# Performance work log

Hardware: AMD Instinct MI355X
Metric: run time of the kernel (lower is better)

## Reference

```python
import jax, jax.numpy as jnp
import numpy as np

HEADS = 8
DIM_HEAD = 64
SCALE = DIM_HEAD ** -0.5


def setup_inputs() -> dict:
    key = jax.random.key(0)
    k1, k2, k3, k4 = jax.random.split(key, 4)
    b, dim, l = 4, 512, 2048
    hidden = HEADS * DIM_HEAD  # 512
    x = jax.random.normal(k1, (b, dim, l), dtype=jnp.float32)
    w_qkv = jax.random.normal(k2, (3 * hidden, dim), dtype=jnp.float32) * (dim ** -0.5)
    w_out = jax.random.normal(k3, (dim, hidden), dtype=jnp.float32) * (hidden ** -0.5)
    b_out = jax.random.normal(k4, (dim,), dtype=jnp.float32) * 0.01
    return {"x": x, "w_qkv": w_qkv, "w_out": w_out, "b_out": b_out}


def reference(x, w_qkv, w_out, b_out):
    b, c, l = x.shape
    h, d = HEADS, DIM_HEAD
    # 1x1 Conv1d == channel matmul: [3*hidden, c] x [b, c, l] -> [b, 3*hidden, l]
    qkv = jnp.einsum('oc,bcl->bol', w_qkv, x)
    q, k, v = jnp.split(qkv, 3, axis=1)
    # 'b (h d) l -> b h d l'
    q = q.reshape(b, h, d, l) * SCALE
    k = k.reshape(b, h, d, l)
    v = v.reshape(b, h, d, l)
    sim = jnp.einsum('bhdi,bhdj->bhij', q, k)          # [b, h, l, l]
    attn = jax.nn.softmax(sim, axis=-1)
    out = jnp.einsum('bhij,bhdj->bhid', attn, v)       # [b, h, l, d]
    # 'b h l d -> b (h d) l'
    out = out.transpose(0, 1, 3, 2).reshape(b, h * d, l)
    return jnp.einsum('oc,bcl->bol', w_out, out) + b_out[None, :, None]
```

## Files before the change

kernel.cpp:

```cpp
#include <hip/hip_runtime.h>

#define L_SEQ 2048
#define KDIM  512

typedef __attribute__((ext_vector_type(8))) short short8v;
typedef __attribute__((ext_vector_type(4))) float f32x4;

static __device__ __forceinline__ short f2b(float f) {
    union { float f; unsigned u; } v; v.f = f;
    unsigned r = v.u + 0x7fffu + ((v.u >> 16) & 1u);
    return (short)(r >> 16);
}

static __device__ __forceinline__ float fast_exp2(float x) {
#if __has_builtin(__builtin_amdgcn_exp2f)
    return __builtin_amdgcn_exp2f(x);
#else
    return exp2f(x);
#endif
}

static __device__ __forceinline__ void gl2lds16(const short* g, short* l) {
    __builtin_amdgcn_global_load_lds(
        (const __attribute__((address_space(1))) unsigned*)g,
        (__attribute__((address_space(3))) unsigned*)l,
        16, 0, 0);
}

__global__ __launch_bounds__(256) void prep(
    const float* __restrict__ wq, const float* __restrict__ wo,
    const float* __restrict__ x,
    short* __restrict__ wqb, short* __restrict__ wob, short* __restrict__ xT)
{
    __shared__ __align__(16) float T[64 * 72];
    const int t = threadIdx.x;
    int bid = blockIdx.x;

    if (bid < 1024) {
        const int i = bid * 256 + t;
        const int NQ = 1536 * 512 / 4;
        float4 v;
        if (i < NQ) v = ((const float4*)wq)[i];
        else        v = ((const float4*)wo)[i - NQ];
        short4 s;
        s.x = f2b(v.x); s.y = f2b(v.y); s.z = f2b(v.z); s.w = f2b(v.w);
        if (i < NQ) ((short4*)wqb)[i] = s;
        else        ((short4*)wob)[i - NQ] = s;
        return;
    }
    bid -= 1024;
    const int l0 = (bid & 31) * 64;
    const int c0 = ((bid >> 5) & 7) * 64;
    const int b  = bid >> 8;

#pragma unroll
    for (int j = 0; j < 4; ++j) {
        const int idx = j * 256 + t;
        const int row = idx >> 4, c4 = idx & 15;
        const float4 v = *(const float4*)&x[((size_t)b * KDIM + c0 + row) * L_SEQ + l0 + c4 * 4];
        *(float4*)&T[row * 72 + c4 * 4] = v;
    }
    __syncthreads();

#pragma unroll
    for (int j = 0; j < 2; ++j) {
        const int idx = j * 256 + t;
        const int l = idx >> 3, ch = idx & 7;
        short8v s;
#pragma unroll
        for (int e = 0; e < 8; ++e)
            s[e] = f2b(T[(ch * 8 + e) * 72 + l]);
        *(short8v*)&xT[((size_t)b * L_SEQ + l0 + l) * KDIM + c0 + ch * 8] = s;
    }
}

template<int EPI>
__global__ __launch_bounds__(256) void gemm_bt(
    const short* __restrict__ Ag, const short* __restrict__ Bbase,
    const float* __restrict__ bias,
    short* __restrict__ Qws, short* __restrict__ Kws, short* __restrict__ Vws,
    float* __restrict__ Cout)
{
    constexpr int TO   = (EPI == 0) ? 128 : 64;
    constexpr int WO   = TO / 2;
    constexpr int NI   = WO / 16;
    constexpr int CA   = TO * 64 * 2 / 1024;
    constexpr int CB   = 16;
    constexpr int CPW  = (CA + CB) / 4;
    constexpr int SMEM = (EPI == 0) ? 34816 : 24576;

    const int bz = blockIdx.z;
    const int o0 = blockIdx.y * TO;
    const int l0 = blockIdx.x * 128;
    const short* Bg = Bbase + (size_t)bz * L_SEQ * KDIM;

    __shared__ __align__(16) char smem[SMEM];
    short* sA = (short*)smem;
    short* sB = (short*)(smem + TO * 64 * 2);

    const int t    = threadIdx.x;
    const int w    = t >> 6;
    const int lane = t & 63;
    const int quad = lane >> 4;
    const int l16  = lane & 15;
    const int wo   = (w & 1) * WO;
    const int wl   = (w >> 1) * 64;

    f32x4 acc[NI][4];
#pragma unroll
    for (int i = 0; i < NI; ++i)
#pragma unroll
        for (int n = 0; n < 4; ++n) acc[i][n] = (f32x4){0,0,0,0};

    const int lrow = lane >> 3;
    const int lcol = (lane & 7) * 8;

    for (int k0 = 0; k0 < KDIM; k0 += 64) {
#pragma unroll
        for (int p = 0; p < CPW; ++p) {
            const int cid = w * CPW + p;
            if (cid < CA) {
                const int row = cid * 8 + lrow;
                gl2lds16(Ag + (size_t)(o0 + row) * KDIM + k0 + lcol, sA + cid * 512);
            } else {
                const int row = (cid - CA) * 8 + lrow;
                gl2lds16(Bg + (size_t)(l0 + row) * KDIM + k0 + lcol, sB + (cid - CA) * 512);
            }
        }
        __syncthreads();

#pragma unroll
        for (int ks = 0; ks < 2; ++ks) {
            short8v af[NI], bf[4];
#pragma unroll
            for (int i = 0; i < NI; ++i)
                af[i] = *(const short8v*)&sA[(wo + i * 16 + l16) * 64 + ks * 32 + quad * 8];
#pragma unroll
            for (int n = 0; n < 4; ++n)
                bf[n] = *(const short8v*)&sB[(wl + n * 16 + l16) * 64 + ks * 32 + quad * 8];
#pragma unroll
            for (int i = 0; i < NI; ++i)
#pragma unroll
                for (int n = 0; n < 4; ++n)
                    acc[i][n] = __builtin_amdgcn_mfma_f32_16x16x32_bf16(af[i], bf[n], acc[i][n], 0, 0, 0);
        }
        __syncthreads();
    }

    if (EPI == 0) {
        const int type  = o0 >> 9;
        const int local = o0 & 511;
        const int bh0   = bz * 8 + (local >> 6);
        const float sc  = (type == 0) ? 0.18033688011112042f : 1.0f;
        short* T = (short*)smem;

        if (type == 2) {
#pragma unroll
            for (int i = 0; i < NI; ++i)
#pragma unroll
                for (int n = 0; n < 4; ++n)
#pragma unroll
                    for (int r = 0; r < 4; ++r)
                        T[(wo + i * 16 + quad * 4 + r) * 136 + wl + n * 16 + l16] =
                            f2b(acc[i][n][r]);
            __syncthreads();
#pragma unroll
            for (int p = 0; p < 8; ++p) {
                const int idx = p * 256 + t;
                const int o = idx >> 4, c = idx & 15;
                const float4 v = *(const float4*)&T[o * 136 + c * 8];
                short* dst = Vws + ((size_t)(bh0 + (o >> 6)) * 64 + (o & 63)) * L_SEQ + l0 + c * 8;
                *(float4*)dst = v;
            }
        } else {
#pragma unroll
            for (int i = 0; i < NI; ++i)
#pragma unroll
                for (int n = 0; n < 4; ++n) {
                    short4 s;
                    s.x = f2b(acc[i][n][0] * sc);
                    s.y = f2b(acc[i][n][1] * sc);
                    s.z = f2b(acc[i][n][2] * sc);
                    s.w = f2b(acc[i][n][3] * sc);
                    *(short4*)&T[(wl + n * 16 + l16) * 136 + wo + i * 16 + quad * 4] = s;
                }
            __syncthreads();
            short* base = (type == 0) ? Qws : Kws;
#pragma unroll
            for (int p = 0; p < 8; ++p) {
                const int idx = p * 256 + t;
                const int l = idx >> 4, c = idx & 15;
                const float4 v = *(const float4*)&T[l * 136 + c * 8];
                short* dst = base + ((size_t)(bh0 + (c >> 3)) * L_SEQ + l0 + l) * 64 + (c & 7) * 8;
                *(float4*)dst = v;
            }
        }
    } else {
        float* Cb = Cout + (size_t)bz * KDIM * L_SEQ;
#pragma unroll
        for (int i = 0; i < NI; ++i) {
            const int o = o0 + wo + i * 16 + quad * 4;
            float bv[4];
#pragma unroll
            for (int r = 0; r < 4; ++r) bv[r] = bias[o + r];
#pragma unroll
            for (int n = 0; n < 4; ++n) {
                const int l = l0 + wl + n * 16 + l16;
#pragma unroll
                for (int r = 0; r < 4; ++r)
                    Cb[(size_t)(o + r) * L_SEQ + l] = acc[i][n][r] + bv[r];
            }
        }
    }
}

__global__ __launch_bounds__(256) void attn_mfma(
    const short* __restrict__ Qws, const short* __restrict__ Kws,
    const short* __restrict__ Vws, short* __restrict__ ao)
{
    const int bh = blockIdx.x & 31;
    const int b  = bh >> 3;
    const int h  = bh & 7;
    const int i0 = (blockIdx.x >> 5) * 128;

    __shared__ __align__(16) char smem[36864];
    short* Kld = (short*)smem;
    short* Vld = (short*)(smem + 9216);
    short* Pld = (short*)(smem + 18432);
    float* Old = (float*)smem;

    const int t    = threadIdx.x;
    const int w    = t >> 6;
    const int lane = t & 63;
    const int quad = lane >> 4;
    const int l16  = lane & 15;

    const short* Qb = Qws + (size_t)bh * L_SEQ * 64;
    const short* Kb = Kws + (size_t)bh * L_SEQ * 64;
    const short* Vb = Vws + (size_t)bh * 64 * L_SEQ;

    short8v qa[2][2];
#pragma unroll
    for (int hh = 0; hh < 2; ++hh) {
        const short* qrow = Qb + (size_t)(i0 + w * 32 + hh * 16 + l16) * 64 + quad * 8;
        qa[hh][0] = *(const short8v*)qrow;
        qa[hh][1] = *(const short8v*)(qrow + 32);
    }

    f32x4 oacc[2][4];
#pragma unroll
    for (int hh = 0; hh < 2; ++hh)
#pragma unroll
        for (int n = 0; n < 4; ++n) oacc[hh][n] = (f32x4){0,0,0,0};
    float rsum[2] = {0.f, 0.f};
    short* Pw = Pld + w * 32 * 72;

    const int r = t >> 2, c = t & 3;

    for (int j0 = 0; j0 < L_SEQ; j0 += 64) {
        {
            const float4 k0 = *(const float4*)(Kb + (size_t)(j0 + r) * 64 + c * 16);
            const float4 k1 = *(const float4*)(Kb + (size_t)(j0 + r) * 64 + c * 16 + 8);
            const float4 v0 = *(const float4*)(Vb + (size_t)r * L_SEQ + j0 + c * 16);
            const float4 v1 = *(const float4*)(Vb + (size_t)r * L_SEQ + j0 + c * 16 + 8);
            *(float4*)&Kld[r * 72 + c * 16]     = k0;
            *(float4*)&Kld[r * 72 + c * 16 + 8] = k1;
            *(float4*)&Vld[r * 72 + c * 16]     = v0;
            *(float4*)&Vld[r * 72 + c * 16 + 8] = v1;
        }
        __syncthreads();

        f32x4 sacc[2][4];
#pragma unroll
        for (int hh = 0; hh < 2; ++hh)
#pragma unroll
            for (int n = 0; n < 4; ++n) sacc[hh][n] = (f32x4){0,0,0,0};
#pragma unroll
        for (int n = 0; n < 4; ++n) {
            short8v kf0 = *(const short8v*)&Kld[(n * 16 + l16) * 72 + quad * 8];
            short8v kf1 = *(const short8v*)&Kld[(n * 16 + l16) * 72 + 32 + quad * 8];
#pragma unroll
            for (int hh = 0; hh < 2; ++hh) {
                sacc[hh][n] = __builtin_amdgcn_mfma_f32_16x16x32_bf16(kf0, qa[hh][0], sacc[hh][n], 0, 0, 0);
                sacc[hh][n] = __builtin_amdgcn_mfma_f32_16x16x32_bf16(kf1, qa[hh][1], sacc[hh][n], 0, 0, 0);
            }
        }

#pragma unroll
        for (int hh = 0; hh < 2; ++hh)
#pragma unroll
            for (int n = 0; n < 4; ++n) {
                const float p0 = fast_exp2(sacc[hh][n][0]);
                const float p1 = fast_exp2(sacc[hh][n][1]);
                const float p2 = fast_exp2(sacc[hh][n][2]);
                const float p3 = fast_exp2(sacc[hh][n][3]);
                rsum[hh] += (p0 + p1) + (p2 + p3);
                uint2 pv;
                pv.x = __builtin_amdgcn_perm(__float_as_uint(p1), __float_as_uint(p0), 0x07060302u);
                pv.y = __builtin_amdgcn_perm(__float_as_uint(p3), __float_as_uint(p2), 0x07060302u);
                *(uint2*)&Pw[(hh * 16 + l16) * 72 + n * 16 + quad * 4] = pv;
            }

        short8v pa[2][2];
#pragma unroll
        for (int hh = 0; hh < 2; ++hh) {
            pa[hh][0] = *(const short8v*)&Pw[(hh * 16 + l16) * 72 + quad * 8];
            pa[hh][1] = *(const short8v*)&Pw[(hh * 16 + l16) * 72 + 32 + quad * 8];
        }
#pragma unroll
        for (int n = 0; n < 4; ++n) {
            short8v vf0 = *(const short8v*)&Vld[(n * 16 + l16) * 72 + quad * 8];
            short8v vf1 = *(const short8v*)&Vld[(n * 16 + l16) * 72 + 32 + quad * 8];
#pragma unroll
            for (int hh = 0; hh < 2; ++hh) {
                oacc[hh][n] = __builtin_amdgcn_mfma_f32_16x16x32_bf16(pa[hh][0], vf0, oacc[hh][n], 0, 0, 0);
                oacc[hh][n] = __builtin_amdgcn_mfma_f32_16x16x32_bf16(pa[hh][1], vf1, oacc[hh][n], 0, 0, 0);
            }
        }
        __syncthreads();
    }

    float inv[2];
#pragma unroll
    for (int hh = 0; hh < 2; ++hh) {
        rsum[hh] += __shfl_xor(rsum[hh], 16, 64);
        rsum[hh] += __shfl_xor(rsum[hh], 32, 64);
        inv[hh] = 1.0014f / rsum[hh];
    }

#pragma unroll
    for (int hh = 0; hh < 2; ++hh)
#pragma unroll
        for (int rr = 0; rr < 4; ++rr) {
            const float iv = __shfl(inv[hh], quad * 4 + rr, 64);
#pragma unroll
            for (int n = 0; n < 4; ++n)
                Old[(w * 32 + hh * 16 + quad * 4 + rr) * 68 + n * 16 + l16] =
                    oacc[hh][n][rr] * iv;
        }
    __syncthreads();
#pragma unroll
    for (int p = 0; p < 8; ++p) {
        const int idx = p * 256 + t;
        const int i = idx >> 4, c4 = idx & 15;
        const float4 v = *(const float4*)&Old[i * 68 + c4 * 4];
        short4 s;
        s.x = f2b(v.x); s.y = f2b(v.y); s.z = f2b(v.z); s.w = f2b(v.w);
        *(short4*)&ao[((size_t)b * L_SEQ + i0 + i) * KDIM + h * 64 + c4 * 4] = s;
    }
}

extern "C" void kernel_launch(void* const* d_in, const int* in_sizes, int n_in,
                              void* d_out, int out_size, void* d_ws, size_t ws_size,
                              hipStream_t stream)
{
    const float* x     = (const float*)d_in[0];
    const float* w_qkv = (const float*)d_in[1];
    const float* w_out = (const float*)d_in[2];
    const float* b_out = (const float*)d_in[3];
    float* out = (float*)d_out;

    char* ws = (char*)d_ws;
    short* xT    = (short*)ws;                      ws += (size_t)4 * L_SEQ * KDIM * 2;
    short* wq_bf = (short*)ws;                      ws += (size_t)1536 * 512 * 2;
    short* wo_bf = (short*)ws;                      ws += (size_t)512 * 512 * 2;
    short* Qws   = (short*)ws;                      ws += (size_t)32 * L_SEQ * 64 * 2;
    short* Kws   = (short*)ws;                      ws += (size_t)32 * L_SEQ * 64 * 2;
    short* Vws   = (short*)ws;                      ws += (size_t)32 * L_SEQ * 64 * 2;
    short* ao    = (short*)ws;

    dim3 blk(256);
    prep       <<<dim3(2048), blk, 0, stream>>>(w_qkv, w_out, x, wq_bf, wo_bf, xT);
    gemm_bt<0> <<<dim3(16, 12, 4), blk, 0, stream>>>(wq_bf, xT, nullptr, Qws, Kws, Vws, nullptr);
    attn_mfma  <<<dim3(512), blk, 0, stream>>>(Qws, Kws, Vws, ao);
    gemm_bt<1> <<<dim3(16, 8, 4), blk, 0, stream>>>(wo_bf, ao, b_out, nullptr, nullptr, nullptr, out);
}
```

Before: 168.1 us.

## Double-buffer K/V tiles and split attention block into eight 16-row waves

The attention kernel now uses 512 threads, with each wave owning 16 query rows instead of 32. K/V tiles are double-buffered in LDS, and the next tile is prefetched into registers while the current one is computed, which leaves one barrier per iteration. This aims to hide global load latency and raise wave-level parallelism per block. The cost is more LDS per block and less K/V fragment reuse per wave, which may lower occupancy.

```diff
diff --git a/kernel.cpp b/kernel.cpp
--- a/kernel.cpp
+++ b/kernel.cpp
@@ -214,7 +214,7 @@
     }
 }
 
-__global__ __launch_bounds__(256) void attn_mfma(
+__global__ __launch_bounds__(512) void attn_mfma(
     const short* __restrict__ Qws, const short* __restrict__ Kws,
     const short* __restrict__ Vws, short* __restrict__ ao)
 {
@@ -223,10 +223,8 @@
     const int h  = bh & 7;
     const int i0 = (blockIdx.x >> 5) * 128;
 
-    __shared__ __align__(16) char smem[36864];
-    short* Kld = (short*)smem;
-    short* Vld = (short*)(smem + 9216);
-    short* Pld = (short*)(smem + 18432);
+    __shared__ __align__(16) char smem[55296];
+    short* Pld = (short*)(smem + 36864);
     float* Old = (float*)smem;
 
     const int t    = threadIdx.x;
@@ -239,109 +237,101 @@
     const short* Kb = Kws + (size_t)bh * L_SEQ * 64;
     const short* Vb = Vws + (size_t)bh * 64 * L_SEQ;
 
-    short8v qa[2][2];
-#pragma unroll
-    for (int hh = 0; hh < 2; ++hh) {
-        const short* qrow = Qb + (size_t)(i0 + w * 32 + hh * 16 + l16) * 64 + quad * 8;
-        qa[hh][0] = *(const short8v*)qrow;
-        qa[hh][1] = *(const short8v*)(qrow + 32);
-    }
-
-    f32x4 oacc[2][4];
-#pragma unroll
-    for (int hh = 0; hh < 2; ++hh)
-#pragma unroll
-        for (int n = 0; n < 4; ++n) oacc[hh][n] = (f32x4){0,0,0,0};
-    float rsum[2] = {0.f, 0.f};
-    short* Pw = Pld + w * 32 * 72;
-
-    const int r = t >> 2, c = t & 3;
-
-    for (int j0 = 0; j0 < L_SEQ; j0 += 64) {
-        {
-            const float4 k0 = *(const float4*)(Kb + (size_t)(j0 + r) * 64 + c * 16);
-            const float4 k1 = *(const float4*)(Kb + (size_t)(j0 + r) * 64 + c * 16 + 8);
-            const float4 v0 = *(const float4*)(Vb + (size_t)r * L_SEQ + j0 + c * 16);
-            const float4 v1 = *(const float4*)(Vb + (size_t)r * L_SEQ + j0 + c * 16 + 8);
-            *(float4*)&Kld[r * 72 + c * 16]     = k0;
-            *(float4*)&Kld[r * 72 + c * 16 + 8] = k1;
-            *(float4*)&Vld[r * 72 + c * 16]     = v0;
-            *(float4*)&Vld[r * 72 + c * 16 + 8] = v1;
+    short8v qa0, qa1;
+    {
+        const short* qrow = Qb + (size_t)(i0 + w * 16 + l16) * 64 + quad * 8;
+        qa0 = *(const short8v*)qrow;
+        qa1 = *(const short8v*)(qrow + 32);
+    }
+
+    f32x4 oacc[4];
+#pragma unroll
+    for (int n = 0; n < 4; ++n) oacc[n] = (f32x4){0,0,0,0};
+    float rsum = 0.f;
+    short* Pw = Pld + w * 16 * 72;
+
+    const int r = t >> 3, c = t & 7;
+
+    {
+        short* K0 = (short*)smem;
+        short* V0 = (short*)(smem + 9216);
+        const float4 k0 = *(const float4*)(Kb + (size_t)r * 64 + c * 8);
+        const float4 v0 = *(const float4*)(Vb + (size_t)r * L_SEQ + c * 8);
+        *(float4*)&K0[r * 72 + c * 8] = k0;
+        *(float4*)&V0[r * 72 + c * 8] = v0;
+    }
+    __syncthreads();
+
+    for (int jt = 0; jt < L_SEQ / 64; ++jt) {
+        const int j0 = jt * 64;
+        short* Kc = (short*)(smem + (jt & 1) * 18432);
+        short* Vc = (short*)(smem + (jt & 1) * 18432 + 9216);
+        const bool more = (jt + 1 < L_SEQ / 64);
+
+        float4 nk, nv;
+        if (more) {
+            nk = *(const float4*)(Kb + (size_t)(j0 + 64 + r) * 64 + c * 8);
+            nv = *(const float4*)(Vb + (size_t)r * L_SEQ + j0 + 64 + c * 8);
+        }
+
+        f32x4 sacc[4];
+#pragma unroll
+        for (int n = 0; n < 4; ++n) sacc[n] = (f32x4){0,0,0,0};
+#pragma unroll
+        for (int n = 0; n < 4; ++n) {
+            const short8v kf0 = *(const short8v*)&Kc[(n * 16 + l16) * 72 + quad * 8];
+            const short8v kf1 = *(const short8v*)&Kc[(n * 16 + l16) * 72 + 32 + quad * 8];
+            sacc[n] = __builtin_amdgcn_mfma_f32_16x16x32_bf16(kf0, qa0, sacc[n], 0, 0, 0);
+            sacc[n] = __builtin_amdgcn_mfma_f32_16x16x32_bf16(kf1, qa1, sacc[n], 0, 0, 0);
+        }
+
+#pragma unroll
+        for (int n = 0; n < 4; ++n) {
+            const float p0 = fast_exp2(sacc[n][0]);
+            const float p1 = fast_exp2(sacc[n][1]);
+            const float p2 = fast_exp2(sacc[n][2]);
+            const float p3 = fast_exp2(sacc[n][3]);
+            rsum += (p0 + p1) + (p2 + p3);
+            uint2 pv;
+            pv.x = __builtin_amdgcn_perm(__float_as_uint(p1), __float_as_uint(p0), 0x07060302u);
+            pv.y = __builtin_amdgcn_perm(__float_as_uint(p3), __float_as_uint(p2), 0x07060302u);
+            *(uint2*)&Pw[l16 * 72 + n * 16 + quad * 4] = pv;
+        }
+
+        const short8v pa0 = *(const short8v*)&Pw[l16 * 72 + quad * 8];
+        const short8v pa1 = *(const short8v*)&Pw[l16 * 72 + 32 + quad * 8];
+#pragma unroll
+        for (int n = 0; n < 4; ++n) {
+            const short8v vf0 = *(const short8v*)&Vc[(n * 16 + l16) * 72 + quad * 8];
+            const short8v vf1 = *(const short8v*)&Vc[(n * 16 + l16) * 72 + 32 + quad * 8];
+            oacc[n] = __builtin_amdgcn_mfma_f32_16x16x32_bf16(pa0, vf0, oacc[n], 0, 0, 0);
+            oacc[n] = __builtin_amdgcn_mfma_f32_16x16x32_bf16(pa1, vf1, oacc[n], 0, 0, 0);
+        }
+
+        if (more) {
+            short* Kn = (short*)(smem + ((jt & 1) ^ 1) * 18432);
+            short* Vn = (short*)(smem + ((jt & 1) ^ 1) * 18432 + 9216);
+            *(float4*)&Kn[r * 72 + c * 8] = nk;
+            *(float4*)&Vn[r * 72 + c * 8] = nv;
         }
         __syncthreads();
-
-        f32x4 sacc[2][4];
-#pragma unroll
-        for (int hh = 0; hh < 2; ++hh)
-#pragma unroll
-            for (int n = 0; n < 4; ++n) sacc[hh][n] = (f32x4){0,0,0,0};
-#pragma unroll
-        for (int n = 0; n < 4; ++n) {
-            short8v kf0 = *(const short8v*)&Kld[(n * 16 + l16) * 72 + quad * 8];
-            short8v kf1 = *(const short8v*)&Kld[(n * 16 + l16) * 72 + 32 + quad * 8];
-#pragma unroll
-            for (int hh = 0; hh < 2; ++hh) {
-                sacc[hh][n] = __builtin_amdgcn_mfma_f32_16x16x32_bf16(kf0, qa[hh][0], sacc[hh][n], 0, 0, 0);
-                sacc[hh][n] = __builtin_amdgcn_mfma_f32_16x16x32_bf16(kf1, qa[hh][1], sacc[hh][n], 0, 0, 0);
-            }
-        }
-
-#pragma unroll
-        for (int hh = 0; hh < 2; ++hh)
-#pragma unroll
-            for (int n = 0; n < 4; ++n) {
-                const float p0 = fast_exp2(sacc[hh][n][0]);
-                const float p1 = fast_exp2(sacc[hh][n][1]);
-                const float p2 = fast_exp2(sacc[hh][n][2]);
-                const float p3 = fast_exp2(sacc[hh][n][3]);
-                rsum[hh] += (p0 + p1) + (p2 + p3);
-                uint2 pv;
-                pv.x = __builtin_amdgcn_perm(__float_as_uint(p1), __float_as_uint(p0), 0x07060302u);
-                pv.y = __builtin_amdgcn_perm(__float_as_uint(p3), __float_as_uint(p2), 0x07060302u);
-                *(uint2*)&Pw[(hh * 16 + l16) * 72 + n * 16 + quad * 4] = pv;
-            }
-
-        short8v pa[2][2];
-#pragma unroll
-        for (int hh = 0; hh < 2; ++hh) {
-            pa[hh][0] = *(const short8v*)&Pw[(hh * 16 + l16) * 72 + quad * 8];
-            pa[hh][1] = *(const short8v*)&Pw[(hh * 16 + l16) * 72 + 32 + quad * 8];
-        }
-#pragma unroll
-        for (int n = 0; n < 4; ++n) {
-            short8v vf0 = *(const short8v*)&Vld[(n * 16 + l16) * 72 + quad * 8];
-            short8v vf1 = *(const short8v*)&Vld[(n * 16 + l16) * 72 + 32 + quad * 8];
-#pragma unroll
-            for (int hh = 0; hh < 2; ++hh) {
-                oacc[hh][n] = __builtin_amdgcn_mfma_f32_16x16x32_bf16(pa[hh][0], vf0, oacc[hh][n], 0, 0, 0);
-                oacc[hh][n] = __builtin_amdgcn_mfma_f32_16x16x32_bf16(pa[hh][1], vf1, oacc[hh][n], 0, 0, 0);
-            }
-        }
-        __syncthreads();
-    }
-
-    float inv[2];
-#pragma unroll
-    for (int hh = 0; hh < 2; ++hh) {
-        rsum[hh] += __shfl_xor(rsum[hh], 16, 64);
-        rsum[hh] += __shfl_xor(rsum[hh], 32, 64);
-        inv[hh] = 1.0014f / rsum[hh];
-    }
-
-#pragma unroll
-    for (int hh = 0; hh < 2; ++hh)
-#pragma unroll
-        for (int rr = 0; rr < 4; ++rr) {
-            const float iv = __shfl(inv[hh], quad * 4 + rr, 64);
-#pragma unroll
-            for (int n = 0; n < 4; ++n)
-                Old[(w * 32 + hh * 16 + quad * 4 + rr) * 68 + n * 16 + l16] =
-                    oacc[hh][n][rr] * iv;
-        }
+    }
+
+    rsum += __shfl_xor(rsum, 16, 64);
+    rsum += __shfl_xor(rsum, 32, 64);
+    const float inv = 1.0014f / rsum;
+
+#pragma unroll
+    for (int rr = 0; rr < 4; ++rr) {
+        const float iv = __shfl(inv, quad * 4 + rr, 64);
+#pragma unroll
+        for (int n = 0; n < 4; ++n)
+            Old[(w * 16 + quad * 4 + rr) * 68 + n * 16 + l16] = oacc[n][rr] * iv;
+    }
     __syncthreads();
 #pragma unroll
-    for (int p = 0; p < 8; ++p) {
-        const int idx = p * 256 + t;
+    for (int p = 0; p < 4; ++p) {
+        const int idx = p * 512 + t;
         const int i = idx >> 4, c4 = idx & 15;
         const float4 v = *(const float4*)&Old[i * 68 + c4 * 4];
         short4 s;
@@ -372,6 +362,6 @@
     dim3 blk(256);
     prep       <<<dim3(2048), blk, 0, stream>>>(w_qkv, w_out, x, wq_bf, wo_bf, xT);
     gemm_bt<0> <<<dim3(16, 12, 4), blk, 0, stream>>>(wq_bf, xT, nullptr, Qws, Kws, Vws, nullptr);
-    attn_mfma  <<<dim3(512), blk, 0, stream>>>(Qws, Kws, Vws, ao);
+    attn_mfma  <<<dim3(512), dim3(512), 0, stream>>>(Qws, Kws, Vws, ao);
     gemm_bt<1> <<<dim3(16, 8, 4), blk, 0, stream>>>(wo_bf, ao, b_out, nullptr, nullptr, nullptr, out);
 }
```

New measurement: 168.8 us. About the same (+0.4%).
